# Performance work log

Measured on AMD Instinct MI355X. Metric: run time of the kernel, lower is better.

Reference implementation:

```python
import jax, jax.numpy as jnp
import numpy as np

CONV_ORDER = 3


def _aggr_norm(L, x):
    # neighborhood_size = row sums of operator; 1/ns with non-finite -> 0
    inv = 1.0 / jnp.sum(L, axis=1)
    inv = jnp.where(jnp.isfinite(inv), inv, 0.0)
    x = inv[:, None] * x
    return jnp.where(jnp.isfinite(x), x, 0.0)


def _chebyshev_conv(L, x, conv_order=CONV_ORDER, aggr_norm=True):
    # Returns [N, C, conv_order]: X[...,k] = norm(L @ X[...,k-1]), X[...,-1 base] = x
    def step(carry, _):
        y = L @ carry
        if aggr_norm:
            y = _aggr_norm(L, y)
        return y, y
    _, X = jax.lax.scan(step, x, None, length=conv_order)  # [K, N, C]
    return jnp.moveaxis(X, 0, -1)  # [N, C, K]


def setup_inputs() -> dict:
    key = jax.random.key(0)
    ks = jax.random.split(key, 13)
    N0, N1, N2, C = 4096, 8192, 4096, 16
    w_scale = 1.414 * np.sqrt(2.0 / (C + C))  # xavier_normal-like
    return {
        "x_0": jax.random.normal(ks[0], (N0, C), jnp.float32),
        "x_1": jax.random.normal(ks[1], (N1, C), jnp.float32),
        "x_2": jax.random.normal(ks[2], (N2, C), jnp.float32),
        "laplacian_0": jax.random.normal(ks[3], (N0, N0), jnp.float32),
        "laplacian_down_1": jax.random.normal(ks[4], (N1, N1), jnp.float32),
        "laplacian_up_1": jax.random.normal(ks[5], (N1, N1), jnp.float32),
        "laplacian_down_2": jax.random.normal(ks[6], (N2, N2), jnp.float32),
        "laplacian_up_2": jax.random.normal(ks[7], (N2, N2), jnp.float32),
        "b1": jax.random.normal(ks[8], (N0, N1), jnp.float32),
        "b2": jax.random.normal(ks[9], (N1, N2), jnp.float32),
        "weight_0": w_scale * jax.random.normal(ks[10], (C, C, 2 + 2 * CONV_ORDER), jnp.float32),
        "weight_1": w_scale * jax.random.normal(ks[11], (C, C, 6 * CONV_ORDER + 3), jnp.float32),
        "weight_2": w_scale * jax.random.normal(ks[12], (C, C, 4 * CONV_ORDER + 2), jnp.float32),
    }


def reference(x_0, x_1, x_2, laplacian_0, laplacian_down_1, laplacian_up_1,
              laplacian_down_2, laplacian_up_2, b1, b2,
              weight_0, weight_1, weight_2):
    # Node-space convolution (the torch forward returns only y_0; the edge/face
    # branches are dead code w.r.t. the returned value and are omitted).
    x_0_lap = _chebyshev_conv(laplacian_0, x_0)                 # [N0, C, K]
    x_0_to_0 = jnp.concatenate([x_0[:, :, None], x_0_lap], axis=2)
    x_1_to_0_upper = b1 @ x_1                                   # [N0, C]
    x_1_to_0_lap = _chebyshev_conv(laplacian_0, x_1_to_0_upper)
    x_1_to_0 = jnp.concatenate([x_1_to_0_upper[:, :, None], x_1_to_0_lap], axis=2)
    x_0_all = jnp.concatenate([x_0_to_0, x_1_to_0], axis=2)     # [N0, C, 2+2K]
    y_0 = jnp.einsum('nik,iok->no', x_0_all, weight_0)
    return y_0
```

## Files before the change

### kernel.cpp

```cpp
#include <hip/hip_runtime.h>
#include <hip/hip_bf16.h>
#include <math.h>

#define N0 4096
#define NM1 8192

template<int NV>
__device__ __forceinline__ void red_scatter(float* v, const int d, const int lane) {
  const bool up = (lane & d) != 0;
  #pragma unroll
  for (int i = 0; i < NV; ++i) {
    float send = up ? v[i] : v[i + NV];
    float recv = __shfl_xor(send, d);
    float keep = up ? v[i + NV] : v[i];
    v[i] = keep + recv;
  }
}

__global__ __launch_bounds__(256)
void b1_matmul_kernel(const float* __restrict__ A,
                      const float* __restrict__ X,
                      float* __restrict__ pP)
{
  __shared__ float4 Bs[2048];
  const int tid  = threadIdx.x;
  const int wv   = tid >> 6;
  const int lane = tid & 63;
  const int q    = lane >> 5;
  const int ml   = lane & 31;
  const int s    = blockIdx.x & 3;
  const int rg   = blockIdx.x >> 2;
  const int row0 = rg * 16 + wv * 4;

  float acc[32];
  #pragma unroll
  for (int i = 0; i < 32; ++i) acc[i] = 0.0f;
  const int j0 = q * 2;
  const int jj = tid & 3;
  const int mt = tid >> 2;

  for (int ch = 0; ch < 4; ++ch) {
    const int mb = s * 2048 + ch * 512;
    __syncthreads();
    #pragma unroll
    for (int k = 0; k < 8; ++k) {
      const int m = mt + 64 * k;
      Bs[(m * 4 + jj) ^ ((m >> 2) & 7)] =
          *(const float4*)(X + (size_t)(mb + m) * 16 + jj * 4);
    }
    __syncthreads();
    #pragma unroll
    for (int it = 0; it < 4; ++it) {
      const int mloc = it * 128 + ml * 4;
      float a[4][4];
      #pragma unroll
      for (int r = 0; r < 4; ++r) {
        const float4 t4 = *(const float4*)(A + (size_t)(row0 + r) * NM1 + mb + mloc);
        a[r][0] = t4.x; a[r][1] = t4.y; a[r][2] = t4.z; a[r][3] = t4.w;
      }
      #pragma unroll
      for (int v = 0; v < 4; ++v) {
        const int mm = mloc + v;
        const int h = (mm >> 2) & 7;
        const float4 b0  = Bs[(mm * 4 + j0) ^ h];
        const float4 b1v = Bs[(mm * 4 + j0 + 1) ^ h];
        #pragma unroll
        for (int r = 0; r < 4; ++r) {
          const float av = a[r][v];
          acc[r*8+0] += av * b0.x;   acc[r*8+1] += av * b0.y;
          acc[r*8+2] += av * b0.z;   acc[r*8+3] += av * b0.w;
          acc[r*8+4] += av * b1v.x;  acc[r*8+5] += av * b1v.y;
          acc[r*8+6] += av * b1v.z;  acc[r*8+7] += av * b1v.w;
        }
      }
    }
  }

  red_scatter<16>(acc, 1, lane);
  red_scatter<8>(acc, 2, lane);
  red_scatter<4>(acc, 4, lane);
  red_scatter<2>(acc, 8, lane);
  red_scatter<1>(acc, 16, lane);

  const int r = 2 * (ml & 1) + ((ml >> 1) & 1);
  const int c = 4 * ((ml >> 2) & 1) + 2 * ((ml >> 3) & 1) + ((ml >> 4) & 1);
  pP[(size_t)(s * N0 + row0 + r) * 16 + q * 8 + c] = acc[0];
}

__global__ void finalize_u_kernel(const float* __restrict__ pP,
                                  float* __restrict__ u) {
  const int idx = blockIdx.x * 256 + threadIdx.x;
  u[idx] = pP[idx] + pP[65536 + idx] + pP[131072 + idx] + pP[196608 + idx];
}

template<bool RS>
__global__ __launch_bounds__(256)
void cheb_step_kernel(const float* __restrict__ A,
                      const float* __restrict__ cx,
                      const float* __restrict__ cu,
                      float* __restrict__ pX,
                      float* __restrict__ pU,
                      float* __restrict__ pRS)
{
  __shared__ float4 Bs[2048];
  const int tid  = threadIdx.x;
  const int wv   = tid >> 6;
  const int lane = tid & 63;
  const int q    = lane >> 4;
  const int ml   = lane & 15;
  const int s    = blockIdx.x & 3;
  const int rg   = blockIdx.x >> 2;
  const int row0 = rg * 16 + wv * 4;

  float acc[32];
  #pragma unroll
  for (int i = 0; i < 32; ++i) acc[i] = 0.0f;
  float rs[4] = {0.0f, 0.0f, 0.0f, 0.0f};
  const int j0 = q * 2;

  const int jj   = tid & 7;
  const int mt   = tid >> 3;
  const float* sbase = (jj < 4) ? cx : cu;
  const int joff = (jj & 3) * 4;

  for (int ch = 0; ch < 4; ++ch) {
    const int mb = s * 1024 + ch * 256;
    __syncthreads();
    #pragma unroll
    for (int k = 0; k < 8; ++k) {
      const int m = mt + 32 * k;
      Bs[(m * 8 + jj) ^ ((m >> 2) & 7)] =
          *(const float4*)(sbase + (size_t)(mb + m) * 16 + joff);
    }
    __syncthreads();
    #pragma unroll
    for (int it = 0; it < 4; ++it) {
      const int mloc = it * 64 + ml * 4;
      float a[4][4];
      #pragma unroll
      for (int r = 0; r < 4; ++r) {
        const float4 t4 = *(const float4*)(A + (size_t)(row0 + r) * N0 + mb + mloc);
        a[r][0] = t4.x; a[r][1] = t4.y; a[r][2] = t4.z; a[r][3] = t4.w;
      }
      #pragma unroll
      for (int v = 0; v < 4; ++v) {
        const int mm = mloc + v;
        const int h = (mm >> 2) & 7;
        const float4 b0  = Bs[(mm * 8 + j0) ^ h];
        const float4 b1v = Bs[(mm * 8 + j0 + 1) ^ h];
        #pragma unroll
        for (int r = 0; r < 4; ++r) {
          const float av = a[r][v];
          acc[r*8+0] += av * b0.x;   acc[r*8+1] += av * b0.y;
          acc[r*8+2] += av * b0.z;   acc[r*8+3] += av * b0.w;
          acc[r*8+4] += av * b1v.x;  acc[r*8+5] += av * b1v.y;
          acc[r*8+6] += av * b1v.z;  acc[r*8+7] += av * b1v.w;
          if constexpr (RS) rs[r] += av;
        }
      }
    }
  }

  red_scatter<16>(acc, 1, lane);
  red_scatter<8>(acc, 2, lane);
  red_scatter<4>(acc, 4, lane);
  red_scatter<2>(acc, 8, lane);

  const int r  = 2 * (ml & 1) + ((ml >> 1) & 1);
  const int cL = 4 * ((ml >> 2) & 1) + 2 * ((ml >> 3) & 1);
  float* base = (q >> 1) ? pU : pX;
  float* dst = base + (size_t)(s * N0 + row0 + r) * 16 + (q & 1) * 8 + cL;
  *(float2*)dst = make_float2(acc[0], acc[1]);

  if constexpr (RS) {
    red_scatter<2>(rs, 1, lane);
    red_scatter<1>(rs, 2, lane);
    float rsum = rs[0] + __shfl_xor(rs[0], 4);
    rsum += __shfl_xor(rsum, 8);
    if (q == 0 && ml < 4) pRS[s * N0 + row0 + r] = rsum;
  }
}

__global__ void norm1_kernel(const float* __restrict__ pX,
                             const float* __restrict__ pU,
                             const float* __restrict__ pRS,
                             float* __restrict__ inv,
                             float* __restrict__ ox,
                             float* __restrict__ ou) {
  const int idx = blockIdx.x * 256 + threadIdx.x;
  const int row = idx >> 4;
  float rsv = pRS[row] + pRS[N0 + row] + pRS[2 * N0 + row] + pRS[3 * N0 + row];
  float iv = 1.0f / rsv;
  if (!isfinite(iv)) iv = 0.0f;
  if ((idx & 15) == 0) inv[row] = iv;
  float xv = (pX[idx] + pX[65536 + idx] + pX[131072 + idx] + pX[196608 + idx]) * iv;
  float uv = (pU[idx] + pU[65536 + idx] + pU[131072 + idx] + pU[196608 + idx]) * iv;
  ox[idx] = isfinite(xv) ? xv : 0.0f;
  ou[idx] = isfinite(uv) ? uv : 0.0f;
}

__global__ void norm23_kernel(const float* __restrict__ pX,
                              const float* __restrict__ pU,
                              const float* __restrict__ inv,
                              float* __restrict__ ox,
                              float* __restrict__ ou) {
  const int idx = blockIdx.x * 256 + threadIdx.x;
  const float iv = inv[idx >> 4];
  float xv = (pX[idx] + pX[65536 + idx] + pX[131072 + idx] + pX[196608 + idx]) * iv;
  float uv = (pU[idx] + pU[65536 + idx] + pU[131072 + idx] + pU[196608 + idx]) * iv;
  ox[idx] = isfinite(xv) ? xv : 0.0f;
  ou[idx] = isfinite(uv) ? uv : 0.0f;
}

__global__ void einsum_kernel(const float* __restrict__ x0,
                              const float* __restrict__ xl1,
                              const float* __restrict__ xl2,
                              const float* __restrict__ u,
                              const float* __restrict__ ul1,
                              const float* __restrict__ ul2,
                              const float* __restrict__ pX,
                              const float* __restrict__ pU,
                              const float* __restrict__ inv,
                              const float* __restrict__ W,
                              float* __restrict__ y) {
  __shared__ float Wl[2048];
  __shared__ float xs[16 * 128];
  const int t = threadIdx.x;
  const int row0 = blockIdx.x * 16;
  #pragma unroll
  for (int k = 0; k < 8; ++k) Wl[t + 256 * k] = W[t + 256 * k];
  const int r = t >> 4;
  const int i = t & 15;
  const int g = (row0 + r) * 16 + i;
  const float iv = inv[row0 + r];
  float x3 = (pX[g] + pX[65536 + g] + pX[131072 + g] + pX[196608 + g]) * iv;
  float u3 = (pU[g] + pU[65536 + g] + pU[131072 + g] + pU[196608 + g]) * iv;
  if (!isfinite(x3)) x3 = 0.0f;
  if (!isfinite(u3)) u3 = 0.0f;
  xs[r * 128 + 0 * 16 + i] = x0[g];
  xs[r * 128 + 1 * 16 + i] = xl1[g];
  xs[r * 128 + 2 * 16 + i] = xl2[g];
  xs[r * 128 + 3 * 16 + i] = x3;
  xs[r * 128 + 4 * 16 + i] = u[g];
  xs[r * 128 + 5 * 16 + i] = ul1[g];
  xs[r * 128 + 6 * 16 + i] = ul2[g];
  xs[r * 128 + 7 * 16 + i] = u3;
  __syncthreads();
  const int o = t & 15;
  float acc = 0.0f;
  #pragma unroll
  for (int ii = 0; ii < 16; ++ii) {
    #pragma unroll
    for (int k = 0; k < 8; ++k)
      acc += xs[r * 128 + k * 16 + ii] * Wl[(ii * 16 + o) * 8 + k];
  }
  y[(row0 + r) * 16 + o] = acc;
}

extern "C" void kernel_launch(void* const* d_in, const int* in_sizes, int n_in,
                              void* d_out, int out_size, void* d_ws, size_t ws_size,
                              hipStream_t stream) {
  const float* x0 = (const float*)d_in[0];
  const float* x1 = (const float*)d_in[1];
  const float* L0 = (const float*)d_in[3];
  const float* B1 = (const float*)d_in[8];
  const float* W0 = (const float*)d_in[10];

  float* ws  = (float*)d_ws;
  float* u   = ws;
  float* xl1 = ws + 65536;
  float* xl2 = ws + 131072;
  float* ul1 = ws + 196608;
  float* ul2 = ws + 262144;
  float* inv = ws + 327680;
  float* pX  = ws + 331776;
  float* pU  = ws + 593920;
  float* pRS = ws + 856064;

  b1_matmul_kernel<<<1024, 256, 0, stream>>>(B1, x1, pX);
  finalize_u_kernel<<<256, 256, 0, stream>>>(pX, u);

  cheb_step_kernel<true><<<1024, 256, 0, stream>>>(L0, x0, u, pX, pU, pRS);
  norm1_kernel<<<256, 256, 0, stream>>>(pX, pU, pRS, inv, xl1, ul1);
  cheb_step_kernel<false><<<1024, 256, 0, stream>>>(L0, xl1, ul1, pX, pU, pRS);
  norm23_kernel<<<256, 256, 0, stream>>>(pX, pU, inv, xl2, ul2);
  cheb_step_kernel<false><<<1024, 256, 0, stream>>>(L0, xl2, ul2, pX, pU, pRS);

  einsum_kernel<<<256, 256, 0, stream>>>(x0, xl1, xl2, u, ul1, ul2,
                                         pX, pU, inv, W0, (float*)d_out);
}
```

Baseline: 136.5 us.

## Retile Chebyshev matvec to 8 rows per wave with 8-way K split; fuse u finalize

The Chebyshev step kernel now has each wave handle 8 rows with one float4 column group per lane, and splits the K dimension 8 ways instead of 4. Each B-tile value loaded from LDS is reused across more rows, and each A value feeds four accumulators. The separate finalize_u kernel is removed: the first cheb step and the einsum sum the four b1 partials on the fly. In exchange, the norm and einsum kernels read twice as many partial buffers and the workspace grows.

```diff
diff --git a/kernel.cpp b/kernel.cpp
--- a/kernel.cpp
+++ b/kernel.cpp
@@ -4,6 +4,16 @@
 
 #define N0 4096
 #define NM1 8192
+
+#define OFF_XL1 0
+#define OFF_XL2 65536
+#define OFF_UL1 131072
+#define OFF_UL2 196608
+#define OFF_INV 262144
+#define OFF_PB  266240
+#define OFF_PX  528384
+#define OFF_PU  1052672
+#define OFF_PRS 1576960
 
 template<int NV>
 __device__ __forceinline__ void red_scatter(float* v, const int d, const int lane) {
@@ -87,74 +97,82 @@
   pP[(size_t)(s * N0 + row0 + r) * 16 + q * 8 + c] = acc[0];
 }
 
-__global__ void finalize_u_kernel(const float* __restrict__ pP,
-                                  float* __restrict__ u) {
-  const int idx = blockIdx.x * 256 + threadIdx.x;
-  u[idx] = pP[idx] + pP[65536 + idx] + pP[131072 + idx] + pP[196608 + idx];
-}
-
-template<bool RS>
+template<bool RS, bool SUMU>
 __global__ __launch_bounds__(256)
-void cheb_step_kernel(const float* __restrict__ A,
-                      const float* __restrict__ cx,
-                      const float* __restrict__ cu,
-                      float* __restrict__ pX,
-                      float* __restrict__ pU,
-                      float* __restrict__ pRS)
+void cheb_kernel(const float* __restrict__ A,
+                 const float* __restrict__ cx,
+                 const float* __restrict__ cu,
+                 float* __restrict__ pX,
+                 float* __restrict__ pU,
+                 float* __restrict__ pRS)
 {
   __shared__ float4 Bs[2048];
   const int tid  = threadIdx.x;
   const int wv   = tid >> 6;
   const int lane = tid & 63;
-  const int q    = lane >> 4;
-  const int ml   = lane & 15;
-  const int s    = blockIdx.x & 3;
-  const int rg   = blockIdx.x >> 2;
-  const int row0 = rg * 16 + wv * 4;
+  const int q    = lane >> 3;
+  const int ml   = lane & 7;
+  const int s    = blockIdx.x & 7;
+  const int rg   = blockIdx.x >> 3;
+  const int row0 = rg * 32 + wv * 8;
+  const int mbase = s * 512;
 
   float acc[32];
   #pragma unroll
   for (int i = 0; i < 32; ++i) acc[i] = 0.0f;
-  float rs[4] = {0.0f, 0.0f, 0.0f, 0.0f};
-  const int j0 = q * 2;
-
-  const int jj   = tid & 7;
-  const int mt   = tid >> 3;
+  float rs[8] = {};
+
+  const int jj = tid & 7;
+  const int mt = tid >> 3;
   const float* sbase = (jj < 4) ? cx : cu;
   const int joff = (jj & 3) * 4;
 
-  for (int ch = 0; ch < 4; ++ch) {
-    const int mb = s * 1024 + ch * 256;
+  #pragma unroll 1
+  for (int ch = 0; ch < 2; ++ch) {
+    const int mb = mbase + ch * 256;
     __syncthreads();
     #pragma unroll
     for (int k = 0; k < 8; ++k) {
       const int m = mt + 32 * k;
-      Bs[(m * 8 + jj) ^ ((m >> 2) & 7)] =
-          *(const float4*)(sbase + (size_t)(mb + m) * 16 + joff);
+      float4 val;
+      if constexpr (SUMU) {
+        if (jj >= 4) {
+          const float* pb = cu + (size_t)(mb + m) * 16 + joff;
+          const float4 t0 = *(const float4*)(pb);
+          const float4 t1 = *(const float4*)(pb + 65536);
+          const float4 t2 = *(const float4*)(pb + 131072);
+          const float4 t3 = *(const float4*)(pb + 196608);
+          val = make_float4(t0.x + t1.x + t2.x + t3.x,
+                            t0.y + t1.y + t2.y + t3.y,
+                            t0.z + t1.z + t2.z + t3.z,
+                            t0.w + t1.w + t2.w + t3.w);
+        } else {
+          val = *(const float4*)(cx + (size_t)(mb + m) * 16 + joff);
+        }
+      } else {
+        val = *(const float4*)(sbase + (size_t)(mb + m) * 16 + joff);
+      }
+      Bs[(m * 8 + jj) ^ ((m >> 2) & 7)] = val;
     }
     __syncthreads();
-    #pragma unroll
-    for (int it = 0; it < 4; ++it) {
-      const int mloc = it * 64 + ml * 4;
-      float a[4][4];
+    #pragma unroll 2
+    for (int it = 0; it < 8; ++it) {
+      const int mloc = it * 32 + ml * 4;
+      float a_[8][4];
       #pragma unroll
-      for (int r = 0; r < 4; ++r) {
+      for (int r = 0; r < 8; ++r) {
         const float4 t4 = *(const float4*)(A + (size_t)(row0 + r) * N0 + mb + mloc);
-        a[r][0] = t4.x; a[r][1] = t4.y; a[r][2] = t4.z; a[r][3] = t4.w;
+        a_[r][0] = t4.x; a_[r][1] = t4.y; a_[r][2] = t4.z; a_[r][3] = t4.w;
       }
       #pragma unroll
       for (int v = 0; v < 4; ++v) {
         const int mm = mloc + v;
-        const int h = (mm >> 2) & 7;
-        const float4 b0  = Bs[(mm * 8 + j0) ^ h];
-        const float4 b1v = Bs[(mm * 8 + j0 + 1) ^ h];
+        const float4 b0 = Bs[(mm * 8 + q) ^ ((mm >> 2) & 7)];
         #pragma unroll
-        for (int r = 0; r < 4; ++r) {
-          const float av = a[r][v];
-          acc[r*8+0] += av * b0.x;   acc[r*8+1] += av * b0.y;
-          acc[r*8+2] += av * b0.z;   acc[r*8+3] += av * b0.w;
-          acc[r*8+4] += av * b1v.x;  acc[r*8+5] += av * b1v.y;
-          acc[r*8+6] += av * b1v.z;  acc[r*8+7] += av * b1v.w;
+        for (int r = 0; r < 8; ++r) {
+          const float av = a_[r][v];
+          acc[r*4+0] += av * b0.x;  acc[r*4+1] += av * b0.y;
+          acc[r*4+2] += av * b0.z;  acc[r*4+3] += av * b0.w;
           if constexpr (RS) rs[r] += av;
         }
       }
@@ -164,20 +182,17 @@
   red_scatter<16>(acc, 1, lane);
   red_scatter<8>(acc, 2, lane);
   red_scatter<4>(acc, 4, lane);
-  red_scatter<2>(acc, 8, lane);
-
-  const int r  = 2 * (ml & 1) + ((ml >> 1) & 1);
-  const int cL = 4 * ((ml >> 2) & 1) + 2 * ((ml >> 3) & 1);
-  float* base = (q >> 1) ? pU : pX;
-  float* dst = base + (size_t)(s * N0 + row0 + r) * 16 + (q & 1) * 8 + cL;
-  *(float2*)dst = make_float2(acc[0], acc[1]);
+
+  const int r = 4 * (ml & 1) + 2 * ((ml >> 1) & 1) + ((ml >> 2) & 1);
+  float* base = (q >> 2) ? pU : pX;
+  *(float4*)(base + (size_t)(s * 65536) + (row0 + r) * 16 + (q & 3) * 4) =
+      make_float4(acc[0], acc[1], acc[2], acc[3]);
 
   if constexpr (RS) {
-    red_scatter<2>(rs, 1, lane);
-    red_scatter<1>(rs, 2, lane);
-    float rsum = rs[0] + __shfl_xor(rs[0], 4);
-    rsum += __shfl_xor(rsum, 8);
-    if (q == 0 && ml < 4) pRS[s * N0 + row0 + r] = rsum;
+    red_scatter<4>(rs, 1, lane);
+    red_scatter<2>(rs, 2, lane);
+    red_scatter<1>(rs, 4, lane);
+    if (q == 0) pRS[s * N0 + row0 + r] = rs[0];
   }
 }
 
@@ -189,12 +204,16 @@
                              float* __restrict__ ou) {
   const int idx = blockIdx.x * 256 + threadIdx.x;
   const int row = idx >> 4;
-  float rsv = pRS[row] + pRS[N0 + row] + pRS[2 * N0 + row] + pRS[3 * N0 + row];
+  float rsv = 0.0f;
+  #pragma unroll
+  for (int s2 = 0; s2 < 8; ++s2) rsv += pRS[s2 * N0 + row];
   float iv = 1.0f / rsv;
   if (!isfinite(iv)) iv = 0.0f;
   if ((idx & 15) == 0) inv[row] = iv;
-  float xv = (pX[idx] + pX[65536 + idx] + pX[131072 + idx] + pX[196608 + idx]) * iv;
-  float uv = (pU[idx] + pU[65536 + idx] + pU[131072 + idx] + pU[196608 + idx]) * iv;
+  float xv = 0.0f, uv = 0.0f;
+  #pragma unroll
+  for (int s2 = 0; s2 < 8; ++s2) { xv += pX[s2*65536 + idx]; uv += pU[s2*65536 + idx]; }
+  xv *= iv; uv *= iv;
   ox[idx] = isfinite(xv) ? xv : 0.0f;
   ou[idx] = isfinite(uv) ? uv : 0.0f;
 }
@@ -206,8 +225,10 @@
                               float* __restrict__ ou) {
   const int idx = blockIdx.x * 256 + threadIdx.x;
   const float iv = inv[idx >> 4];
-  float xv = (pX[idx] + pX[65536 + idx] + pX[131072 + idx] + pX[196608 + idx]) * iv;
-  float uv = (pU[idx] + pU[65536 + idx] + pU[131072 + idx] + pU[196608 + idx]) * iv;
+  float xv = 0.0f, uv = 0.0f;
+  #pragma unroll
+  for (int s2 = 0; s2 < 8; ++s2) { xv += pX[s2*65536 + idx]; uv += pU[s2*65536 + idx]; }
+  xv *= iv; uv *= iv;
   ox[idx] = isfinite(xv) ? xv : 0.0f;
   ou[idx] = isfinite(uv) ? uv : 0.0f;
 }
@@ -215,7 +236,7 @@
 __global__ void einsum_kernel(const float* __restrict__ x0,
                               const float* __restrict__ xl1,
                               const float* __restrict__ xl2,
-                              const float* __restrict__ u,
+                              const float* __restrict__ pB,
                               const float* __restrict__ ul1,
                               const float* __restrict__ ul2,
                               const float* __restrict__ pX,
@@ -233,33 +254,37 @@
   const int i = t & 15;
   const int g = (row0 + r) * 16 + i;
   const float iv = inv[row0 + r];
-  float x3 = (pX[g] + pX[65536 + g] + pX[131072 + g] + pX[196608 + g]) * iv;
-  float u3 = (pU[g] + pU[65536 + g] + pU[131072 + g] + pU[196608 + g]) * iv;
+  float x3 = 0.0f, u3 = 0.0f;
+  #pragma unroll
+  for (int s2 = 0; s2 < 8; ++s2) { x3 += pX[s2*65536 + g]; u3 += pU[s2*65536 + g]; }
+  x3 *= iv; u3 *= iv;
   if (!isfinite(x3)) x3 = 0.0f;
   if (!isfinite(u3)) u3 = 0.0f;
-  xs[r * 128 + 0 * 16 + i] = x0[g];
-  xs[r * 128 + 1 * 16 + i] = xl1[g];
-  xs[r * 128 + 2 * 16 + i] = xl2[g];
-  xs[r * 128 + 3 * 16 + i] = x3;
-  xs[r * 128 + 4 * 16 + i] = u[g];
-  xs[r * 128 + 5 * 16 + i] = ul1[g];
-  xs[r * 128 + 6 * 16 + i] = ul2[g];
-  xs[r * 128 + 7 * 16 + i] = u3;
+  const float uval = pB[g] + pB[65536 + g] + pB[131072 + g] + pB[196608 + g];
+  xs[r*128 + 0*16 + i] = x0[g];
+  xs[r*128 + 1*16 + i] = xl1[g];
+  xs[r*128 + 2*16 + i] = xl2[g];
+  xs[r*128 + 3*16 + i] = x3;
+  xs[r*128 + 4*16 + i] = uval;
+  xs[r*128 + 5*16 + i] = ul1[g];
+  xs[r*128 + 6*16 + i] = ul2[g];
+  xs[r*128 + 7*16 + i] = u3;
   __syncthreads();
   const int o = t & 15;
-  float acc = 0.0f;
+  float a = 0.0f;
   #pragma unroll
   for (int ii = 0; ii < 16; ++ii) {
     #pragma unroll
     for (int k = 0; k < 8; ++k)
-      acc += xs[r * 128 + k * 16 + ii] * Wl[(ii * 16 + o) * 8 + k];
-  }
-  y[(row0 + r) * 16 + o] = acc;
+      a += xs[r*128 + k*16 + ii] * Wl[(ii*16 + o)*8 + k];
+  }
+  y[(row0 + r) * 16 + o] = a;
 }
 
 extern "C" void kernel_launch(void* const* d_in, const int* in_sizes, int n_in,
                               void* d_out, int out_size, void* d_ws, size_t ws_size,
                               hipStream_t stream) {
+  (void)in_sizes; (void)n_in; (void)out_size; (void)ws_size;
   const float* x0 = (const float*)d_in[0];
   const float* x1 = (const float*)d_in[1];
   const float* L0 = (const float*)d_in[3];
@@ -267,25 +292,24 @@
   const float* W0 = (const float*)d_in[10];
 
   float* ws  = (float*)d_ws;
-  float* u   = ws;
-  float* xl1 = ws + 65536;
-  float* xl2 = ws + 131072;
-  float* ul1 = ws + 196608;
-  float* ul2 = ws + 262144;
-  float* inv = ws + 327680;
-  float* pX  = ws + 331776;
-  float* pU  = ws + 593920;
-  float* pRS = ws + 856064;
-
-  b1_matmul_kernel<<<1024, 256, 0, stream>>>(B1, x1, pX);
-  finalize_u_kernel<<<256, 256, 0, stream>>>(pX, u);
-
-  cheb_step_kernel<true><<<1024, 256, 0, stream>>>(L0, x0, u, pX, pU, pRS);
+  float* xl1 = ws + OFF_XL1;
+  float* xl2 = ws + OFF_XL2;
+  float* ul1 = ws + OFF_UL1;
+  float* ul2 = ws + OFF_UL2;
+  float* inv = ws + OFF_INV;
+  float* pB  = ws + OFF_PB;
+  float* pX  = ws + OFF_PX;
+  float* pU  = ws + OFF_PU;
+  float* pRS = ws + OFF_PRS;
+
+  b1_matmul_kernel<<<1024, 256, 0, stream>>>(B1, x1, pB);
+
+  cheb_kernel<true, true><<<1024, 256, 0, stream>>>(L0, x0, pB, pX, pU, pRS);
   norm1_kernel<<<256, 256, 0, stream>>>(pX, pU, pRS, inv, xl1, ul1);
-  cheb_step_kernel<false><<<1024, 256, 0, stream>>>(L0, xl1, ul1, pX, pU, pRS);
+  cheb_kernel<false, false><<<1024, 256, 0, stream>>>(L0, xl1, ul1, pX, pU, pRS);
   norm23_kernel<<<256, 256, 0, stream>>>(pX, pU, inv, xl2, ul2);
-  cheb_step_kernel<false><<<1024, 256, 0, stream>>>(L0, xl2, ul2, pX, pU, pRS);
-
-  einsum_kernel<<<256, 256, 0, stream>>>(x0, xl1, xl2, u, ul1, ul2,
+  cheb_kernel<false, false><<<1024, 256, 0, stream>>>(L0, xl2, ul2, pX, pU, pRS);
+
+  einsum_kernel<<<256, 256, 0, stream>>>(x0, xl1, xl2, pB, ul1, ul2,
                                          pX, pU, inv, W0, (float*)d_out);
 }
```

New measurement: 134.5 us. Within noise of the previous version (-1.4%).
